# Kernel optimization log

Hardware: AMD Instinct MI355X
Metric: run time of the kernel (lower is better)

Reference implementation:

```python
import jax, jax.numpy as jnp
import numpy as np

SEG = 512        # seg_len
REUSE = 2        # reuse_seg_num
D = 512          # d_model
K = 512          # k_dim
NL = 6           # layers per encoder
NSEG = 8         # number of segments (context 4096)
VOCAB = 10000
FF = 2048
MEM = REUSE * SEG


def sinusoid_pos_encode(length, dim):
    pos = jnp.arange(length, dtype=jnp.float32)[:, None]
    idx = jnp.arange(0, dim, 2, dtype=jnp.float32)
    ang = pos / jnp.power(10000.0, idx / dim)
    pe = jnp.zeros((length, dim), dtype=jnp.float32)
    pe = pe.at[:, 0::2].set(jnp.sin(ang))
    pe = pe.at[:, 1::2].set(jnp.cos(ang))
    return pe


def layernorm(x, g, b, eps=1e-5):
    mu = jnp.mean(x, axis=-1, keepdims=True)
    var = jnp.mean(jnp.square(x - mu), axis=-1, keepdims=True)
    return (x - mu) * jax.lax.rsqrt(var + eps) * g + b


def run_encoder(tokens, emb, Wqkvr, Wo, W1, W2, ln, uv):
    # tokens: (NSEG*SEG,) int
    segs = tokens.reshape(NSEG, SEG)
    R = jnp.flip(sinusoid_pos_encode(MEM + SEG, K), axis=0)  # flipped rel. encoding
    u, v = uv[0], uv[1]                                       # (K,), (K,)
    scale = 1.0 / np.sqrt(K)

    def step(prev, xs):
        seg, seg_idx = xs
        state = emb[seg]                                      # (SEG, D)
        # memory validity mask: only the last min(seg_idx, REUSE) segments are real
        n_valid = jnp.minimum(seg_idx, REUSE) * SEG
        mem_bias = jnp.where(jnp.arange(MEM) >= MEM - n_valid, 0.0, -1e9)
        bias = jnp.concatenate([mem_bias, jnp.zeros(SEG)])    # (MEM+SEG,)
        recs = []
        for j in range(NL):
            recs.append(state)
            mem = prev[:, j].reshape(MEM, D)                  # (MEM, D)
            Wq, Wk, Wv, Wr = Wqkvr[j]                         # each (D, K)
            q = state @ Wq                                    # (SEG, K)
            full = jnp.concatenate([mem, state], axis=0)      # (MEM+SEG, D)
            k = full @ Wk
            val = full @ Wv
            pk = R @ Wr                                       # (MEM+SEG, K)
            scores = ((q + u) @ k.T + (q + v) @ pk.T) * scale + bias[None, :]
            attn = jax.nn.softmax(scores, axis=-1)            # (SEG, MEM+SEG)
            out = (attn @ val) @ Wo[j]                        # (SEG, D)
            h = layernorm(state + out, ln[j, 0], ln[j, 1])
            ff = jax.nn.relu(h @ W1[j]) @ W2[j]
            state = layernorm(h + ff, ln[j, 2], ln[j, 3])
        # shift memory: drop oldest, append pre-layer states of this segment
        prev_new = jnp.concatenate([prev[1:], jnp.stack(recs)[None]], axis=0)
        return prev_new, state

    prev0 = jnp.zeros((REUSE, NL, SEG, D), dtype=jnp.float32)
    _, outs = jax.lax.scan(step, prev0, (segs, jnp.arange(NSEG)))
    return outs.reshape(-1, D)  # (NSEG*SEG, D)


def setup_inputs() -> dict:
    key = jax.random.key(0)
    ks = jax.random.split(key, 16)
    s = 0.02
    def mk(k, shape):
        return jax.random.normal(k, shape, dtype=jnp.float32) * s
    inp = {
        "src": jax.random.randint(ks[0], (1, NSEG * SEG), 0, VOCAB, dtype=jnp.int32),
        "pad_idx": 0,
        "emb": mk(ks[1], (VOCAB, D)),
        "Wqkvr_a": mk(ks[2], (NL, 4, D, K)),
        "Wo_a": mk(ks[3], (NL, K, D)),
        "W1_a": mk(ks[4], (NL, D, FF)),
        "W2_a": mk(ks[5], (NL, FF, D)),
        "ln_a": jnp.tile(jnp.array([1.0, 0.0, 1.0, 0.0], dtype=jnp.float32)[None, :, None], (NL, 1, D)),
        "uv_a": jax.random.normal(ks[6], (2, K), dtype=jnp.float32),
        "Wqkvr_b": mk(ks[7], (NL, 4, D, K)),
        "Wo_b": mk(ks[8], (NL, K, D)),
        "W1_b": mk(ks[9], (NL, D, FF)),
        "W2_b": mk(ks[10], (NL, FF, D)),
        "ln_b": jnp.tile(jnp.array([1.0, 0.0, 1.0, 0.0], dtype=jnp.float32)[None, :, None], (NL, 1, D)),
        "uv_b": jax.random.normal(ks[11], (2, K), dtype=jnp.float32),
    }
    return inp


def reference(src, pad_idx, emb, Wqkvr_a, Wo_a, W1_a, W2_a, ln_a, uv_a,
              Wqkvr_b, Wo_b, W1_b, W2_b, ln_b, uv_b):
    tokens = src[0]
    fwd = run_encoder(tokens, emb, Wqkvr_a, Wo_a, W1_a, W2_a, ln_a, uv_a)
    rev = run_encoder(tokens[::-1], emb, Wqkvr_b, Wo_b, W1_b, W2_b, ln_b, uv_b)
    rev = rev[::-1]
    return jnp.concatenate([fwd, rev], axis=-1)  # (NSEG*SEG, 2*D)
```

## Files before the change

kernel.cpp:

```cpp
#include <hip/hip_runtime.h>

typedef __bf16 bf16;
typedef __bf16 bf16x8 __attribute__((ext_vector_type(8)));
typedef __bf16 bf16x4 __attribute__((ext_vector_type(4)));
typedef float f32x4 __attribute__((ext_vector_type(4)));

typedef __attribute__((address_space(3))) void lds_void_t;
typedef const __attribute__((address_space(1))) void gbl_void_t;

#define TOK 4096
#define KBROWS 5120

enum { M_BF16 = 0, M_F32 = 1, M_RELU = 2, M_QKV = 3, M_SCOREXP = 4, M_PV = 5 };

struct GemmArgs {
  const bf16* A; long long sAe, sAi; int ldA;
  const bf16* B; long long sBe, sBi; int ldB;
  const bf16* B2; long long sB2e; int ldB2;
  bf16* C; float* Cf; long long sCe, sCi; int ldC;
  int M, N, K, iPerE;
  bf16 *quv, *kbuf, *vt;
  const float *uvA, *uvB;
  float scale;
};

template<int MODE, bool SPLITB, int TM, int TN>
__global__ __launch_bounds__(256, 4)
void gemm_kernel(GemmArgs g) {
  constexpr int FA = TM / 32, FB = TN / 32;
  int z = blockIdx.z;
  int e = z / g.iPerE;
  int i = z % g.iPerE;
  const bf16* A = g.A + e * g.sAe + i * g.sAi;
  const bf16* B = g.B + e * g.sBe + i * g.sBi;
  const bf16* B2 = nullptr;
  if constexpr (SPLITB) B2 = g.B2 + e * g.sB2e;

  int tm = blockIdx.x * TM;
  int tn = blockIdx.y * TN;

  __shared__ uint4 As4[TM * 8];
  __shared__ uint4 Bs4[TN * 8];
  __shared__ float ls[MODE == M_PV ? TM : 1];
  bf16* As_lds = (bf16*)As4;
  bf16* Bs_lds = (bf16*)Bs4;

  int tid = threadIdx.x;
  int wave = tid >> 6, lane = tid & 63;
  int wm = (wave >> 1) * (TM / 2), wn = (wave & 1) * (TN / 2);
  int quad = lane >> 4, l15 = lane & 15;
  int l7 = l15 & 7;
  int l8r = lane >> 3, l8c = lane & 7;
  int fc = l8c ^ l8r;

  f32x4 acc[FA][FB] = {};
  float lreg[FA];
#pragma unroll
  for (int t = 0; t < FA; ++t) lreg[t] = 0.f;

  for (int k0 = 0; k0 < g.K; k0 += 64) {
#pragma unroll
    for (int ii = 0; ii < FA; ++ii) {
      int rowbase = (wave * FA + ii) * 8;
      int r = rowbase + l8r;
      const bf16* gp = &A[(long long)(tm + r) * g.ldA + k0 + fc * 8];
      __builtin_amdgcn_global_load_lds((gbl_void_t*)gp, (lds_void_t*)&As_lds[rowbase * 64], 16, 0, 0);
    }
#pragma unroll
    for (int ii = 0; ii < FB; ++ii) {
      int rowbase = (wave * FB + ii) * 8;
      int r = rowbase + l8r;
      const bf16* gp;
      if constexpr (SPLITB) {
        int kk = k0 + fc * 8;
        gp = (kk < 512) ? &B[(long long)(tn + r) * g.ldB + kk]
                        : &B2[(long long)(tn + r) * g.ldB2 + (kk - 512)];
      } else {
        gp = &B[(long long)(tn + r) * g.ldB + k0 + fc * 8];
      }
      __builtin_amdgcn_global_load_lds((gbl_void_t*)gp, (lds_void_t*)&Bs_lds[rowbase * 64], 16, 0, 0);
    }
    __syncthreads();
#pragma unroll
    for (int s = 0; s < 2; ++s) {
      int sw = (s * 4 + quad) ^ l7;
      bf16x8 af[FA], bfr[FB];
#pragma unroll
      for (int t = 0; t < FA; ++t) af[t]  = ((const bf16x8*)As4)[(wm + t * 16 + l15) * 8 + sw];
#pragma unroll
      for (int t = 0; t < FB; ++t) bfr[t] = ((const bf16x8*)Bs4)[(wn + t * 16 + l15) * 8 + sw];
      if constexpr (MODE == M_PV) {
#pragma unroll
        for (int t = 0; t < FA; ++t)
#pragma unroll
          for (int q2 = 0; q2 < 8; ++q2) lreg[t] += (float)af[t][q2];
      }
#pragma unroll
      for (int a = 0; a < FA; ++a)
#pragma unroll
        for (int b = 0; b < FB; ++b)
          acc[a][b] = __builtin_amdgcn_mfma_f32_16x16x32_bf16(af[a], bfr[b], acc[a][b], 0, 0, 0);
    }
    __syncthreads();
  }

  if constexpr (MODE == M_PV) {
#pragma unroll
    for (int t = 0; t < FA; ++t) {
      lreg[t] += __shfl_xor(lreg[t], 16);
      lreg[t] += __shfl_xor(lreg[t], 32);
      if (quad == 0) ls[wm + t * 16 + l15] = lreg[t];
    }
    __syncthreads();
  }

  if constexpr (MODE == M_QKV) {
    const float* uv = e ? g.uvB : g.uvA;
#pragma unroll
    for (int a = 0; a < FA; ++a) {
      int mB = tm + wm + a * 16 + quad * 4;
#pragma unroll
      for (int b = 0; b < FB; ++b) {
        int col = tn + wn + b * 16 + l15;
        int region = col >> 9, cin = col & 511;
        float u0 = 0.f, v0 = 0.f;
        if (region == 0) { u0 = uv[cin]; v0 = uv[512 + cin]; }
#pragma unroll
        for (int r = 0; r < 4; ++r) {
          int m = mB + r;
          float val = acc[a][b][r];
          if (region == 0) {
            long long qb = (long long)e * TOK * 1024 + (long long)m * 1024;
            g.quv[qb + cin]       = (bf16)(val + u0);
            g.quv[qb + 512 + cin] = (bf16)(val + v0);
          } else if (region == 1) {
            g.kbuf[(long long)e * KBROWS * 512 + (long long)(1024 + m) * 512 + cin] = (bf16)val;
          } else {
            g.vt[(long long)e * 512 * KBROWS + (long long)cin * KBROWS + 1024 + m] = (bf16)val;
          }
        }
      }
    }
  } else if constexpr (MODE == M_SCOREXP) {
    bf16* C = g.C + e * g.sCe + i * g.sCi;
    int T = 1024 - ((i < 2 ? i : 2) << 9);
#pragma unroll
    for (int a = 0; a < FA; ++a) {
      int mB = tm + wm + a * 16 + quad * 4;
#pragma unroll
      for (int b = 0; b < FB; ++b) {
        int col = tn + wn + b * 16 + l15;
        float bias = (col < T) ? -1e9f : 0.0f;
#pragma unroll
        for (int r = 0; r < 4; ++r)
          C[(long long)(mB + r) * g.ldC + col] = (bf16)__expf(acc[a][b][r] * g.scale + bias);
      }
    }
  } else if constexpr (MODE == M_PV) {
    float* Cf = g.Cf + e * g.sCe + i * g.sCi;
#pragma unroll
    for (int a = 0; a < FA; ++a) {
      int lrow = wm + a * 16 + quad * 4;
      int mB = tm + lrow;
#pragma unroll
      for (int b = 0; b < FB; ++b) {
        int col = tn + wn + b * 16 + l15;
#pragma unroll
        for (int r = 0; r < 4; ++r)
          Cf[(long long)(mB + r) * g.ldC + col] = acc[a][b][r] / ls[lrow + r];
      }
    }
  } else {
#pragma unroll
    for (int a = 0; a < FA; ++a) {
      int mB = tm + wm + a * 16 + quad * 4;
#pragma unroll
      for (int b = 0; b < FB; ++b) {
        int col = tn + wn + b * 16 + l15;
#pragma unroll
        for (int r = 0; r < 4; ++r) {
          float val = acc[a][b][r];
          if constexpr (MODE == M_RELU) val = val > 0.f ? val : 0.f;
          if constexpr (MODE == M_F32) {
            float* Cf = g.Cf + e * g.sCe + i * g.sCi;
            Cf[(long long)(mB + r) * g.ldC + col] = val;
          } else {
            bf16* C = g.C + e * g.sCe + i * g.sCi;
            C[(long long)(mB + r) * g.ldC + col] = (bf16)val;
          }
        }
      }
    }
  }
}

__global__ __launch_bounds__(256)
void prep_weights(const float* qa, const float* qb, const float* oa, const float* ob,
                  const float* w1a, const float* w1b, const float* w2a, const float* w2b,
                  bf16* wqkvT, bf16* wrT, bf16* wvPlain, bf16* woT, bf16* w1T, bf16* w2T) {
  int id = blockIdx.x;
  const float* src; bf16* dst; int R, C, tx, ty; bool plain = false;
  if (id < 3072) {
    int mat = id >> 6, tile = id & 63;
    tx = tile & 7; ty = tile >> 3;
    int e = mat / 24, rj = mat % 24, j = rj >> 2, c = rj & 3;
    src = (e ? qb : qa) + (long long)(j * 4 + c) * 262144;
    R = 512; C = 512;
    if (c < 2)        dst = wqkvT + ((long long)(e * 6 + j) * 3 + c) * 262144;
    else if (c == 2) { dst = wvPlain + (long long)(e * 6 + j) * 262144; plain = true; }
    else              dst = wrT + (long long)(e * 6 + j) * 262144;
  } else if (id < 3840) {
    int id2 = id - 3072; int mat = id2 >> 6, tile = id2 & 63;
    tx = tile & 7; ty = tile >> 3;
    int e = mat / 6, j = mat % 6;
    src = (e ? ob : oa) + (long long)j * 262144;
    dst = woT + (long long)mat * 262144; R = 512; C = 512;
  } else if (id < 6912) {
    int id2 = id - 3840; int mat = id2 >> 8, tile = id2 & 255;
    tx = tile & 31; ty = tile >> 5;
    int e = mat / 6, j = mat % 6;
    src = (e ? w1b : w1a) + (long long)j * 512 * 2048;
    dst = w1T + (long long)mat * 512 * 2048; R = 512; C = 2048;
  } else {
    int id2 = id - 6912; int mat = id2 >> 8, tile = id2 & 255;
    tx = tile & 7; ty = tile >> 3;
    int e = mat / 6, j = mat % 6;
    src = (e ? w2b : w2a) + (long long)j * 2048 * 512;
    dst = w2T + (long long)mat * 2048 * 512; R = 2048; C = 512;
  }
  int c0 = tx * 64, r0 = ty * 64;
  int tid = threadIdx.x;

  if (plain) {
    int c8 = (tid & 7) * 8;
    int r8 = tid >> 3;
#pragma unroll
    for (int rep = 0; rep < 2; ++rep) {
      int rr = r8 + rep * 32;
      const float* sp = &src[(long long)(r0 + rr) * C + c0 + c8];
      float4 f0 = *(const float4*)sp;
      float4 f1 = *(const float4*)(sp + 4);
      bf16 o[8] __attribute__((aligned(16))) =
        {(bf16)f0.x, (bf16)f0.y, (bf16)f0.z, (bf16)f0.w,
         (bf16)f1.x, (bf16)f1.y, (bf16)f1.z, (bf16)f1.w};
      *(bf16x8*)&dst[(long long)(r0 + rr) * C + c0 + c8] = *(const bf16x8*)o;
    }
  } else {
    __shared__ bf16 t[64 * 68];
    int l15 = tid & 15;
    int hi  = tid >> 4;
    int cc = l15 * 4;
#pragma unroll
    for (int rep = 0; rep < 4; ++rep) {
      int rr = hi + rep * 16;
      float4 f = *(const float4*)&src[(long long)(r0 + rr) * C + c0 + cc];
      float v[4] = {f.x, f.y, f.z, f.w};
#pragma unroll
      for (int i2 = 0; i2 < 4; ++i2) {
        int row = cc + i2;
        int col = rr ^ (((row >> 4) & 3) << 2);
        t[row * 68 + col] = (bf16)v[i2];
      }
    }
    __syncthreads();
    int oc = tid >> 2;
    int kk = tid & 3;
    bf16 outv[16] __attribute__((aligned(16)));
#pragma unroll
    for (int u = 0; u < 4; ++u) {
      int col = (16 * kk + 4 * u) ^ (((oc >> 4) & 3) << 2);
      *(bf16x4*)&outv[u * 4] = *(const bf16x4*)&t[oc * 68 + col];
    }
    bf16* dp = &dst[(long long)(c0 + oc) * R + r0 + 16 * kk];
    *(bf16x8*)dp       = *(const bf16x8*)&outv[0];
    *(bf16x8*)(dp + 8) = *(const bf16x8*)&outv[8];
  }
}

__global__ __launch_bounds__(256)
void sinusoid_kernel(bf16* rb) {
  int i = blockIdx.x, m = threadIdx.x;
  float p = (float)(1535 - i);
  float inv = expf(-((float)(2 * m) * (1.0f / 512.0f)) * 9.210340371976184f);
  float ang = p * inv;
  rb[(long long)i * 512 + 2 * m]     = (bf16)sinf(ang);
  rb[(long long)i * 512 + 2 * m + 1] = (bf16)cosf(ang);
}

__global__ __launch_bounds__(128)
void embed_kernel(const int* src, const float* emb, bf16* Sb, float* Sf) {
  int row = blockIdx.x, e = blockIdx.y, tid = threadIdx.x;
  int tok = e ? src[4095 - row] : src[row];
  long long base = ((long long)e * TOK + row) * 512 + tid * 4;
  float4 f = *(const float4*)&emb[(long long)tok * 512 + tid * 4];
  *(float4*)&Sf[base] = f;
  Sb[base + 0] = (bf16)f.x; Sb[base + 1] = (bf16)f.y;
  Sb[base + 2] = (bf16)f.z; Sb[base + 3] = (bf16)f.w;
}

__global__ __launch_bounds__(256)
void zero_kv(bf16* kbuf, bf16* vwoT) {
  int r = blockIdx.x, e = blockIdx.y, which = blockIdx.z, tid = threadIdx.x;
  if (which == 0) {
    bf16* p = kbuf + ((long long)e * KBROWS + r) * 512;
    p[tid] = (bf16)0.f; p[tid + 256] = (bf16)0.f;
  } else if (r < 512) {
    bf16* p = vwoT + ((long long)e * 512 + r) * KBROWS;
#pragma unroll
    for (int k = 0; k < 4; ++k) p[tid + k * 256] = (bf16)0.f;
  }
}

__global__ __launch_bounds__(64)
void ln_kernel(const float* Xf, const float* Tf, const float* lnA, const float* lnB,
               int gOff, bf16* OutB, float* OutF, int outMode, float* finalOut) {
  int row = blockIdx.x, e = blockIdx.y;
  long long base = ((long long)e * TOK + row) * 512;
  const float* x = Xf + base;
  const float* t = Tf + base;
  const float* ln = e ? lnB : lnA;
  const float* gm = ln + gOff;
  const float* bt = ln + gOff + 512;
  int lane = threadIdx.x;
  float vals[8];
  float s = 0.f;
#pragma unroll
  for (int k = 0; k < 8; ++k) { int d = lane + k * 64; vals[k] = x[d] + t[d]; s += vals[k]; }
  for (int off = 32; off; off >>= 1) s += __shfl_xor(s, off);
  float mu = s * (1.0f / 512.0f);
  float vs = 0.f;
#pragma unroll
  for (int k = 0; k < 8; ++k) { float d0 = vals[k] - mu; vs += d0 * d0; }
  for (int off = 32; off; off >>= 1) vs += __shfl_xor(vs, off);
  float rstd = rsqrtf(vs * (1.0f / 512.0f) + 1e-5f);
  if (outMode == 0) {
#pragma unroll
    for (int k = 0; k < 8; ++k) {
      int d = lane + k * 64;
      float y = (vals[k] - mu) * rstd * gm[d] + bt[d];
      OutB[base + d] = (bf16)y;
      OutF[base + d] = y;
    }
  } else {
    long long ob = e ? ((long long)(4095 - row) * 1024 + 512) : ((long long)row * 1024);
#pragma unroll
    for (int k = 0; k < 8; ++k) {
      int d = lane + k * 64;
      finalOut[ob + d] = (vals[k] - mu) * rstd * gm[d] + bt[d];
    }
  }
}

extern "C" void kernel_launch(void* const* d_in, const int* in_sizes, int n_in,
                              void* d_out, int out_size, void* d_ws, size_t ws_size,
                              hipStream_t stream) {
  const int*   src   = (const int*)d_in[0];
  const float* emb   = (const float*)d_in[2];
  const float* Wq_a  = (const float*)d_in[3];
  const float* Wo_a  = (const float*)d_in[4];
  const float* W1_a  = (const float*)d_in[5];
  const float* W2_a  = (const float*)d_in[6];
  const float* ln_a  = (const float*)d_in[7];
  const float* uv_a  = (const float*)d_in[8];
  const float* Wq_b  = (const float*)d_in[9];
  const float* Wo_b  = (const float*)d_in[10];
  const float* W1_b  = (const float*)d_in[11];
  const float* W2_b  = (const float*)d_in[12];
  const float* ln_b  = (const float*)d_in[13];
  const float* uv_b  = (const float*)d_in[14];
  float* out = (float*)d_out;

  char* w = (char*)d_ws;
  size_t off = 0;
  auto alloc = [&](long long elems, int esz) -> char* {
    char* p = w + off;
    off += (size_t)elems * esz;
    off = (off + 255) & ~(size_t)255;
    return p;
  };
  bf16* wqkvT = (bf16*)alloc(2LL * 6 * 1536 * 512, 2);
  bf16* woT   = (bf16*)alloc(2LL * 6 * 512 * 512, 2);
  bf16* w1T   = (bf16*)alloc(2LL * 6 * 2048 * 512, 2);
  bf16* w2T   = (bf16*)alloc(2LL * 6 * 512 * 2048, 2);
  bf16* pk    = (bf16*)alloc(2LL * 6 * 1536 * 512, 2);
  bf16* Sb    = (bf16*)alloc(2LL * TOK * 512, 2);
  float* Sf   = (float*)alloc(2LL * TOK * 512, 4);
  bf16* quv   = (bf16*)alloc(2LL * TOK * 1024, 2);
  bf16* kbuf  = (bf16*)alloc(2LL * KBROWS * 512, 2);
  bf16* vwoT  = (bf16*)alloc(2LL * 512 * KBROWS, 2);
  bf16* P     = (bf16*)alloc(2LL * 8 * 512 * 1536, 2);
  float* t1f  = (float*)alloc(2LL * TOK * 512, 4);
  bf16* f1    = (bf16*)alloc(2LL * TOK * 2048, 2);
  bf16* rb      = f1;
  bf16* wrT     = f1 + 1024LL * 1024;
  bf16* wvPlain = f1 + 4096LL * 1024;

  if (off > ws_size) return;

  prep_weights<<<9984, 256, 0, stream>>>(Wq_a, Wq_b, Wo_a, Wo_b, W1_a, W1_b, W2_a, W2_b,
                                         wqkvT, wrT, wvPlain, woT, w1T, w2T);
  sinusoid_kernel<<<1536, 256, 0, stream>>>(rb);
  embed_kernel<<<dim3(4096, 2), 128, 0, stream>>>(src, emb, Sb, Sf);
  zero_kv<<<dim3(1024, 2, 2), 256, 0, stream>>>(kbuf, vwoT);

  {
    GemmArgs g = {};
    g.A = rb; g.sAe = 0; g.sAi = 0; g.ldA = 512;
    g.B = wrT; g.sBe = 0; g.sBi = 512LL * 512; g.ldB = 512;
    g.C = pk; g.sCe = 0; g.sCi = 1536LL * 512; g.ldC = 512;
    g.M = 1536; g.N = 512; g.K = 512; g.iPerE = 12;
    gemm_kernel<M_BF16, false, 128, 128><<<dim3(12, 4, 12), 256, 0, stream>>>(g);
  }
  {
    GemmArgs g = {};
    g.A = woT; g.sAe = 6LL * 262144; g.sAi = 262144; g.ldA = 512;
    g.B = wvPlain; g.sBe = 6LL * 262144; g.sBi = 262144; g.ldB = 512;
    g.C = wqkvT + 2LL * 262144; g.sCe = 18LL * 262144; g.sCi = 3LL * 262144; g.ldC = 512;
    g.M = 512; g.N = 512; g.K = 512; g.iPerE = 6;
    gemm_kernel<M_BF16, false, 128, 128><<<dim3(4, 4, 12), 256, 0, stream>>>(g);
  }

  const float scale = 0.044194173824159216f;

  for (int j = 0; j < 6; ++j) {
    {
      GemmArgs g = {};
      g.A = Sb; g.sAe = (long long)TOK * 512; g.sAi = 0; g.ldA = 512;
      g.B = wqkvT + (long long)j * 1536 * 512; g.sBe = 6LL * 1536 * 512; g.sBi = 0; g.ldB = 512;
      g.M = TOK; g.N = 1536; g.K = 512; g.iPerE = 1;
      g.quv = quv; g.kbuf = kbuf; g.vt = vwoT; g.uvA = uv_a; g.uvB = uv_b;
      gemm_kernel<M_QKV, false, 128, 128><<<dim3(32, 12, 2), 256, 0, stream>>>(g);
    }
    {
      GemmArgs g = {};
      g.A = quv; g.sAe = (long long)TOK * 1024; g.sAi = 512LL * 1024; g.ldA = 1024;
      g.B = kbuf; g.sBe = (long long)KBROWS * 512; g.sBi = 512LL * 512; g.ldB = 512;
      g.B2 = pk + (long long)j * 1536 * 512; g.sB2e = 6LL * 1536 * 512; g.ldB2 = 512;
      g.C = P; g.sCe = 8LL * 512 * 1536; g.sCi = 512LL * 1536; g.ldC = 1536;
      g.M = 512; g.N = 1536; g.K = 1024; g.iPerE = 8;
      g.scale = scale;
      gemm_kernel<M_SCOREXP, true, 128, 128><<<dim3(4, 12, 16), 256, 0, stream>>>(g);
    }
    {
      GemmArgs g = {};
      g.A = P; g.sAe = 8LL * 512 * 1536; g.sAi = 512LL * 1536; g.ldA = 1536;
      g.B = vwoT; g.sBe = 512LL * KBROWS; g.sBi = 512; g.ldB = KBROWS;
      g.Cf = t1f; g.sCe = (long long)TOK * 512; g.sCi = 512LL * 512; g.ldC = 512;
      g.M = 512; g.N = 512; g.K = 1536; g.iPerE = 8;
      gemm_kernel<M_PV, false, 64, 128><<<dim3(8, 4, 16), 256, 0, stream>>>(g);
    }
    ln_kernel<<<dim3(4096, 2), 64, 0, stream>>>(Sf, t1f, ln_a, ln_b, (j * 4 + 0) * 512, Sb, Sf, 0, out);
    {
      GemmArgs g = {};
      g.A = Sb; g.sAe = (long long)TOK * 512; g.sAi = 0; g.ldA = 512;
      g.B = w1T + (long long)j * 2048 * 512; g.sBe = 6LL * 2048 * 512; g.sBi = 0; g.ldB = 512;
      g.C = f1; g.sCe = (long long)TOK * 2048; g.sCi = 0; g.ldC = 2048;
      g.M = TOK; g.N = 2048; g.K = 512; g.iPerE = 1;
      gemm_kernel<M_RELU, false, 128, 128><<<dim3(32, 16, 2), 256, 0, stream>>>(g);
    }
    {
      GemmArgs g = {};
      g.A = f1; g.sAe = (long long)TOK * 2048; g.sAi = 0; g.ldA = 2048;
      g.B = w2T + (long long)j * 512 * 2048; g.sBe = 6LL * 512 * 2048; g.sBi = 0; g.ldB = 2048;
      g.Cf = t1f; g.sCe = (long long)TOK * 512; g.sCi = 0; g.ldC = 512;
      g.M = TOK; g.N = 512; g.K = 2048; g.iPerE = 1;
      gemm_kernel<M_F32, false, 64, 128><<<dim3(64, 4, 2), 256, 0, stream>>>(g);
    }
    ln_kernel<<<dim3(4096, 2), 64, 0, stream>>>(Sf, t1f, ln_a, ln_b, (j * 4 + 2) * 512, Sb, Sf,
                                                (j == 5) ? 1 : 0, out);
  }
}
```

Baseline: 1.281 ms.

## Vectorize auxiliary kernels and process two tiles per weight-prep block

The weight-prep kernel now handles two adjacent 64x64 tiles per block, issuing all global loads before the conversions and halving the grid. The sinusoid, embed, zero and layernorm kernels switch from scalar bf16/float accesses to packed vector loads and stores, with layernorm lanes owning contiguous 8-element chunks. This targets memory-transaction overhead in the small auxiliary kernels, at the cost of more registers and LDS per prep block. The GEMMs, which dominate runtime, are untouched.

```diff
diff --git a/kernel.cpp b/kernel.cpp
--- a/kernel.cpp
+++ b/kernel.cpp
@@ -3,6 +3,7 @@
 typedef __bf16 bf16;
 typedef __bf16 bf16x8 __attribute__((ext_vector_type(8)));
 typedef __bf16 bf16x4 __attribute__((ext_vector_type(4)));
+typedef __bf16 bf16x2 __attribute__((ext_vector_type(2)));
 typedef float f32x4 __attribute__((ext_vector_type(4)));
 
 typedef __attribute__((address_space(3))) void lds_void_t;
@@ -194,12 +195,15 @@
   }
 }
 
-__global__ __launch_bounds__(256)
-void prep_weights(const float* qa, const float* qb, const float* oa, const float* ob,
-                  const float* w1a, const float* w1b, const float* w2a, const float* w2b,
-                  bf16* wqkvT, bf16* wrT, bf16* wvPlain, bf16* woT, bf16* w1T, bf16* w2T) {
-  int id = blockIdx.x;
-  const float* src; bf16* dst; int R, C, tx, ty; bool plain = false;
+__device__ inline void prep_locate(int id, const float* qa, const float* qb,
+                                   const float* oa, const float* ob,
+                                   const float* w1a, const float* w1b,
+                                   const float* w2a, const float* w2b,
+                                   bf16* wqkvT, bf16* wrT, bf16* wvPlain, bf16* woT,
+                                   bf16* w1T, bf16* w2T,
+                                   const float*& src, bf16*& dst, int& R, int& C,
+                                   int& tx, int& ty, bool& plain) {
+  plain = false;
   if (id < 3072) {
     int mat = id >> 6, tile = id & 63;
     tx = tile & 7; ty = tile >> 3;
@@ -228,52 +232,87 @@
     src = (e ? w2b : w2a) + (long long)j * 2048 * 512;
     dst = w2T + (long long)mat * 2048 * 512; R = 2048; C = 512;
   }
-  int c0 = tx * 64, r0 = ty * 64;
+}
+
+__global__ __launch_bounds__(256)
+void prep_weights(const float* qa, const float* qb, const float* oa, const float* ob,
+                  const float* w1a, const float* w1b, const float* w2a, const float* w2b,
+                  bf16* wqkvT, bf16* wrT, bf16* wvPlain, bf16* woT, bf16* w1T, bf16* w2T) {
+  int id0 = blockIdx.x * 2;
+  const float* src; bf16* dst; int R, C, tx0, ty; bool plain;
+  prep_locate(id0, qa, qb, oa, ob, w1a, w1b, w2a, w2b,
+              wqkvT, wrT, wvPlain, woT, w1T, w2T, src, dst, R, C, tx0, ty, plain);
+  int r0 = ty * 64;
   int tid = threadIdx.x;
 
   if (plain) {
     int c8 = (tid & 7) * 8;
     int r8 = tid >> 3;
-#pragma unroll
-    for (int rep = 0; rep < 2; ++rep) {
-      int rr = r8 + rep * 32;
-      const float* sp = &src[(long long)(r0 + rr) * C + c0 + c8];
-      float4 f0 = *(const float4*)sp;
-      float4 f1 = *(const float4*)(sp + 4);
-      bf16 o[8] __attribute__((aligned(16))) =
-        {(bf16)f0.x, (bf16)f0.y, (bf16)f0.z, (bf16)f0.w,
-         (bf16)f1.x, (bf16)f1.y, (bf16)f1.z, (bf16)f1.w};
-      *(bf16x8*)&dst[(long long)(r0 + rr) * C + c0 + c8] = *(const bf16x8*)o;
+    float4 f[2][4];
+#pragma unroll
+    for (int p = 0; p < 2; ++p) {
+      int c0 = (tx0 + p) * 64;
+#pragma unroll
+      for (int rep = 0; rep < 2; ++rep) {
+        const float* sp = &src[(long long)(r0 + r8 + rep * 32) * C + c0 + c8];
+        f[p][rep * 2]     = *(const float4*)sp;
+        f[p][rep * 2 + 1] = *(const float4*)(sp + 4);
+      }
+    }
+#pragma unroll
+    for (int p = 0; p < 2; ++p) {
+      int c0 = (tx0 + p) * 64;
+#pragma unroll
+      for (int rep = 0; rep < 2; ++rep) {
+        float4 f0 = f[p][rep * 2], f1 = f[p][rep * 2 + 1];
+        bf16 o[8] __attribute__((aligned(16))) =
+          {(bf16)f0.x, (bf16)f0.y, (bf16)f0.z, (bf16)f0.w,
+           (bf16)f1.x, (bf16)f1.y, (bf16)f1.z, (bf16)f1.w};
+        *(bf16x8*)&dst[(long long)(r0 + r8 + rep * 32) * C + c0 + c8] = *(const bf16x8*)o;
+      }
     }
   } else {
-    __shared__ bf16 t[64 * 68];
+    __shared__ bf16 t[2][64 * 68];
     int l15 = tid & 15;
     int hi  = tid >> 4;
     int cc = l15 * 4;
-#pragma unroll
-    for (int rep = 0; rep < 4; ++rep) {
-      int rr = hi + rep * 16;
-      float4 f = *(const float4*)&src[(long long)(r0 + rr) * C + c0 + cc];
-      float v[4] = {f.x, f.y, f.z, f.w};
-#pragma unroll
-      for (int i2 = 0; i2 < 4; ++i2) {
-        int row = cc + i2;
-        int col = rr ^ (((row >> 4) & 3) << 2);
-        t[row * 68 + col] = (bf16)v[i2];
-      }
-    }
+    float4 f[2][4];
+#pragma unroll
+    for (int p = 0; p < 2; ++p) {
+      int c0 = (tx0 + p) * 64;
+#pragma unroll
+      for (int rep = 0; rep < 4; ++rep)
+        f[p][rep] = *(const float4*)&src[(long long)(r0 + hi + rep * 16) * C + c0 + cc];
+    }
+#pragma unroll
+    for (int p = 0; p < 2; ++p)
+#pragma unroll
+      for (int rep = 0; rep < 4; ++rep) {
+        int rr = hi + rep * 16;
+        float v[4] = {f[p][rep].x, f[p][rep].y, f[p][rep].z, f[p][rep].w};
+#pragma unroll
+        for (int i2 = 0; i2 < 4; ++i2) {
+          int row = cc + i2;
+          int col = rr ^ (((row >> 4) & 3) << 2);
+          t[p][row * 68 + col] = (bf16)v[i2];
+        }
+      }
     __syncthreads();
     int oc = tid >> 2;
     int kk = tid & 3;
-    bf16 outv[16] __attribute__((aligned(16)));
-#pragma unroll
-    for (int u = 0; u < 4; ++u) {
-      int col = (16 * kk + 4 * u) ^ (((oc >> 4) & 3) << 2);
-      *(bf16x4*)&outv[u * 4] = *(const bf16x4*)&t[oc * 68 + col];
-    }
-    bf16* dp = &dst[(long long)(c0 + oc) * R + r0 + 16 * kk];
-    *(bf16x8*)dp       = *(const bf16x8*)&outv[0];
-    *(bf16x8*)(dp + 8) = *(const bf16x8*)&outv[8];
+#pragma unroll
+    for (int p = 0; p < 2; ++p) {
+      int c0 = (tx0 + p) * 64;
+      bf16 outv[16] __attribute__((aligned(16)));
+#pragma unroll
+      for (int u = 0; u < 4; ++u) {
+        int col = (16 * kk + 4 * u) ^ (((oc >> 4) & 3) << 2);
+        *(bf16x4*)&outv[u * 4] = *(const bf16x4*)&t[p][oc * 68 + col];
+      }
+      bf16* dp = &dst[(long long)(c0 + oc) * R + r0 + 16 * kk];
+      *(bf16x8*)dp       = *(const bf16x8*)&outv[0];
+      *(bf16x8*)(dp + 8) = *(const bf16x8*)&outv[8];
+    }
   }
 }
 
@@ -283,8 +322,8 @@
   float p = (float)(1535 - i);
   float inv = expf(-((float)(2 * m) * (1.0f / 512.0f)) * 9.210340371976184f);
   float ang = p * inv;
-  rb[(long long)i * 512 + 2 * m]     = (bf16)sinf(ang);
-  rb[(long long)i * 512 + 2 * m + 1] = (bf16)cosf(ang);
+  bf16x2 v = {(bf16)sinf(ang), (bf16)cosf(ang)};
+  *(bf16x2*)&rb[(long long)i * 512 + 2 * m] = v;
 }
 
 __global__ __launch_bounds__(128)
@@ -294,20 +333,18 @@
   long long base = ((long long)e * TOK + row) * 512 + tid * 4;
   float4 f = *(const float4*)&emb[(long long)tok * 512 + tid * 4];
   *(float4*)&Sf[base] = f;
-  Sb[base + 0] = (bf16)f.x; Sb[base + 1] = (bf16)f.y;
-  Sb[base + 2] = (bf16)f.z; Sb[base + 3] = (bf16)f.w;
+  bf16 o[4] __attribute__((aligned(8))) = {(bf16)f.x, (bf16)f.y, (bf16)f.z, (bf16)f.w};
+  *(bf16x4*)&Sb[base] = *(const bf16x4*)o;
 }
 
 __global__ __launch_bounds__(256)
 void zero_kv(bf16* kbuf, bf16* vwoT) {
   int r = blockIdx.x, e = blockIdx.y, which = blockIdx.z, tid = threadIdx.x;
+  uint4 z = {0u, 0u, 0u, 0u};
   if (which == 0) {
-    bf16* p = kbuf + ((long long)e * KBROWS + r) * 512;
-    p[tid] = (bf16)0.f; p[tid + 256] = (bf16)0.f;
+    if (tid < 64) ((uint4*)(kbuf + ((long long)e * KBROWS + r) * 512))[tid] = z;
   } else if (r < 512) {
-    bf16* p = vwoT + ((long long)e * 512 + r) * KBROWS;
-#pragma unroll
-    for (int k = 0; k < 4; ++k) p[tid + k * 256] = (bf16)0.f;
+    if (tid < 128) ((uint4*)(vwoT + ((long long)e * 512 + r) * KBROWS))[tid] = z;
   }
 }
 
@@ -316,38 +353,47 @@
                int gOff, bf16* OutB, float* OutF, int outMode, float* finalOut) {
   int row = blockIdx.x, e = blockIdx.y;
   long long base = ((long long)e * TOK + row) * 512;
-  const float* x = Xf + base;
-  const float* t = Tf + base;
   const float* ln = e ? lnB : lnA;
-  const float* gm = ln + gOff;
-  const float* bt = ln + gOff + 512;
   int lane = threadIdx.x;
-  float vals[8];
+  int d0 = lane * 8;
+  float4 x0 = *(const float4*)&Xf[base + d0];
+  float4 x1 = *(const float4*)&Xf[base + d0 + 4];
+  float4 t0 = *(const float4*)&Tf[base + d0];
+  float4 t1 = *(const float4*)&Tf[base + d0 + 4];
+  float vals[8] = {x0.x + t0.x, x0.y + t0.y, x0.z + t0.z, x0.w + t0.w,
+                   x1.x + t1.x, x1.y + t1.y, x1.z + t1.z, x1.w + t1.w};
   float s = 0.f;
 #pragma unroll
-  for (int k = 0; k < 8; ++k) { int d = lane + k * 64; vals[k] = x[d] + t[d]; s += vals[k]; }
+  for (int k = 0; k < 8; ++k) s += vals[k];
   for (int off = 32; off; off >>= 1) s += __shfl_xor(s, off);
   float mu = s * (1.0f / 512.0f);
   float vs = 0.f;
 #pragma unroll
-  for (int k = 0; k < 8; ++k) { float d0 = vals[k] - mu; vs += d0 * d0; }
+  for (int k = 0; k < 8; ++k) { float d = vals[k] - mu; vs += d * d; }
   for (int off = 32; off; off >>= 1) vs += __shfl_xor(vs, off);
   float rstd = rsqrtf(vs * (1.0f / 512.0f) + 1e-5f);
+  float4 g0 = *(const float4*)&ln[gOff + d0];
+  float4 g1 = *(const float4*)&ln[gOff + d0 + 4];
+  float4 b0 = *(const float4*)&ln[gOff + 512 + d0];
+  float4 b1 = *(const float4*)&ln[gOff + 512 + d0 + 4];
+  float gm[8] = {g0.x, g0.y, g0.z, g0.w, g1.x, g1.y, g1.z, g1.w};
+  float bt[8] = {b0.x, b0.y, b0.z, b0.w, b1.x, b1.y, b1.z, b1.w};
+  float y[8];
+#pragma unroll
+  for (int k = 0; k < 8; ++k) y[k] = (vals[k] - mu) * rstd * gm[k] + bt[k];
   if (outMode == 0) {
-#pragma unroll
-    for (int k = 0; k < 8; ++k) {
-      int d = lane + k * 64;
-      float y = (vals[k] - mu) * rstd * gm[d] + bt[d];
-      OutB[base + d] = (bf16)y;
-      OutF[base + d] = y;
-    }
+    bf16 ob8[8] __attribute__((aligned(16)));
+#pragma unroll
+    for (int k = 0; k < 8; ++k) ob8[k] = (bf16)y[k];
+    *(bf16x8*)&OutB[base + d0] = *(const bf16x8*)ob8;
+    float4 ya = {y[0], y[1], y[2], y[3]}, yb = {y[4], y[5], y[6], y[7]};
+    *(float4*)&OutF[base + d0]     = ya;
+    *(float4*)&OutF[base + d0 + 4] = yb;
   } else {
     long long ob = e ? ((long long)(4095 - row) * 1024 + 512) : ((long long)row * 1024);
-#pragma unroll
-    for (int k = 0; k < 8; ++k) {
-      int d = lane + k * 64;
-      finalOut[ob + d] = (vals[k] - mu) * rstd * gm[d] + bt[d];
-    }
+    float4 ya = {y[0], y[1], y[2], y[3]}, yb = {y[4], y[5], y[6], y[7]};
+    *(float4*)&finalOut[ob + d0]     = ya;
+    *(float4*)&finalOut[ob + d0 + 4] = yb;
   }
 }
 
@@ -397,7 +443,7 @@
 
   if (off > ws_size) return;
 
-  prep_weights<<<9984, 256, 0, stream>>>(Wq_a, Wq_b, Wo_a, Wo_b, W1_a, W1_b, W2_a, W2_b,
+  prep_weights<<<4992, 256, 0, stream>>>(Wq_a, Wq_b, Wo_a, Wo_b, W1_a, W1_b, W2_a, W2_b,
                                          wqkvT, wrT, wvPlain, woT, w1T, w2T);
   sinusoid_kernel<<<1536, 256, 0, stream>>>(rb);
   embed_kernel<<<dim3(4096, 2), 128, 0, stream>>>(src, emb, Sb, Sf);
```

Result: no change. 1.275 ms (-0.5%).
